# Optimization experiments

Hardware: AMD Instinct MI355X
Metric: run time of the kernel (lower is better)

Reference implementation:

```python
import jax, jax.numpy as jnp
import numpy as np

B, H, WD, C = 16, 96, 96, 256
WS, SH, NH = 6, 3, 8
N = WS * WS
ALPHA = (2 * 6) ** 0.25  # deepnorm alpha, n_layers=6
SCALE = (C // NH) ** 0.5  # faithful to source: head_dim**0.5 (not **-0.5)
EPS = 1e-5


def _rel_index(ws):
    coords = np.stack(np.meshgrid(np.arange(ws), np.arange(ws), indexing='ij'))  # (2,ws,ws)
    flat = coords.reshape(2, -1)
    rel = (flat[:, :, None] - flat[:, None, :]).transpose(1, 2, 0).copy()
    rel[..., 0] += ws - 1
    rel[..., 1] += ws - 1
    rel[..., 0] *= 2 * ws - 1
    return jnp.asarray(rel.sum(-1))  # (N,N) int


def _attn_mask(h, w, ws, sh):
    img = np.zeros((h, w))
    cnt = 0
    for hs in (slice(0, -ws), slice(-ws, -sh), slice(-sh, None)):
        for wsl in (slice(0, -ws), slice(-ws, -sh), slice(-sh, None)):
            img[hs, wsl] = cnt
            cnt += 1
    win = img.reshape(h // ws, ws, w // ws, ws).transpose(0, 2, 1, 3).reshape(-1, ws * ws)
    diff = win[:, None, :] - win[:, :, None]
    return jnp.asarray(np.where(diff != 0, -100.0, 0.0), jnp.float32)  # (nW,N,N)


def _ln(t, w, b):
    mu = jnp.mean(t, -1, keepdims=True)
    var = jnp.var(t, -1, keepdims=True)
    return (t - mu) * jax.lax.rsqrt(var + EPS) * w + b


def setup_inputs() -> dict:
    key = jax.random.key(0)
    ks = jax.random.split(key, 8)
    d = {
        'x': jax.random.normal(ks[0], (B, H * WD, C), jnp.float32),
        'qkv_w': jax.random.normal(ks[1], (C, 3 * C), jnp.float32) * 0.02,
        'qkv_b': jnp.zeros((3 * C,), jnp.float32),
        'bias_table': jax.random.normal(ks[2], ((2 * WS - 1) ** 2, NH), jnp.float32) * 0.02,
        'proj_w': jax.random.normal(ks[3], (C, C), jnp.float32) * 0.02,
        'proj_b': jnp.zeros((C,), jnp.float32),
        'norm1_w': jnp.ones((C,), jnp.float32),
        'norm1_b': jnp.zeros((C,), jnp.float32),
        'norm2_w': jnp.ones((C,), jnp.float32),
        'norm2_b': jnp.zeros((C,), jnp.float32),
        'fc1_w': jax.random.normal(ks[4], (C, 4 * C), jnp.float32) * 0.02,
        'fc1_b': jnp.zeros((4 * C,), jnp.float32),
        'fc2_w': jax.random.normal(ks[5], (4 * C, C), jnp.float32) * 0.02,
        'fc2_b': jnp.zeros((C,), jnp.float32),
    }
    return d


def reference(x, qkv_w, qkv_b, bias_table, proj_w, proj_b, norm1_w, norm1_b,
              norm2_w, norm2_b, fc1_w, fc1_b, fc2_w, fc2_b):
    hd = C // NH
    nW = (H // WS) * (WD // WS)
    shortcut = x  # (B, L, C), norm_before=False -> post-norm
    xs = x.reshape(B, H, WD, C)
    xs = jnp.roll(xs, (-SH, -SH), axis=(1, 2))  # cyclic shift
    # window partition -> (B*nW, N, C)
    xw = xs.reshape(B, H // WS, WS, WD // WS, WS, C).transpose(0, 1, 3, 2, 4, 5).reshape(B * nW, N, C)
    qkv = (xw @ qkv_w + qkv_b).reshape(B * nW, N, 3, NH, hd).transpose(2, 0, 3, 1, 4)
    q, k, v = qkv[0] * SCALE, qkv[1], qkv[2]
    attn = jnp.einsum('bhnd,bhmd->bhnm', q, k)  # (B*nW, H, N, N)
    bias = bias_table[_rel_index(WS).reshape(-1)].reshape(N, N, NH).transpose(2, 0, 1)
    attn = attn + bias[None]
    mask = _attn_mask(H, WD, WS, SH)  # (nW, N, N)
    attn = attn.reshape(B, nW, NH, N, N) + mask[None, :, None]
    attn = jax.nn.softmax(attn.reshape(B * nW, NH, N, N), axis=-1)
    out = jnp.einsum('bhnm,bhmd->bhnd', attn, v).transpose(0, 2, 1, 3).reshape(B * nW, N, C)
    out = out @ proj_w + proj_b
    # faithful buggy window_reverse: identity permute == plain reshape
    xs = out.reshape(B, H // WS, WS, WD // WS, WS, C).reshape(B, H, WD, C)
    xs = jnp.roll(xs, (SH, SH), axis=(1, 2))
    x1 = _ln(shortcut * ALPHA + xs.reshape(B, H * WD, C), norm1_w, norm1_b)
    hmid = jax.nn.gelu(x1 @ fc1_w + fc1_b, approximate=False)
    x2 = _ln(x1 * ALPHA + (hmid @ fc2_w + fc2_b), norm2_w, norm2_b)
    return x2
```

## Files before the change

kernel.cpp:

```cpp
#include <hip/hip_runtime.h>
#include <math.h>

typedef __bf16 bf16x8 __attribute__((ext_vector_type(8)));
typedef float f32x4 __attribute__((ext_vector_type(4)));

#define NTOK 147456
#define LTOK 9216
#define ALPHA 1.8612097182041991f
#define QSCALE 5.656854249492380196f
#define MFMA16(a,b,c) __builtin_amdgcn_mfma_f32_16x16x32_bf16((a),(b),(c),0,0,0)
#define SWB(row,kb) ((kb) ^ ((row)&7))

__device__ __forceinline__ float gelu_sig(float x) {
    const float e = __expf(-1.702f * x);
    return x * __builtin_amdgcn_rcpf(1.0f + e);
}

__device__ __forceinline__ void gll16(const void* g, void* l) {
    __builtin_amdgcn_global_load_lds(
        (const __attribute__((address_space(1))) void*)g,
        (__attribute__((address_space(3))) void*)l, 16, 0, 0);
}

__global__ __launch_bounds__(256) void k0_prep(
    const float* __restrict__ qkv_w, const float* __restrict__ proj_w,
    const float* __restrict__ fc1_w, const float* __restrict__ fc2_w,
    __bf16* __restrict__ qkvT, __bf16* __restrict__ projT,
    __bf16* __restrict__ w1T, __bf16* __restrict__ w2T)
{
    const int id = blockIdx.x * 256 + threadIdx.x;
    if (id < 196608) {
        const int o = id >> 8, k = id & 255;
        qkvT[id] = (__bf16)qkv_w[k * 768 + o];
    } else if (id < 262144) {
        const int i = id - 196608, o = i >> 8, k = i & 255;
        projT[i] = (__bf16)proj_w[k * 256 + o];
    } else if (id < 524288) {
        const int i = id - 262144, o = i >> 8, k = i & 255;
        w1T[i] = (__bf16)fc1_w[k * 1024 + o];
    } else {
        const int i = id - 524288, o = i >> 10, k = i & 1023;
        w2T[i] = (__bf16)fc2_w[k * 256 + o];
    }
}

__global__ __launch_bounds__(512, 4) void k1f_qkv_attn(
    const float* __restrict__ x, const __bf16* __restrict__ qkvT,
    const float* __restrict__ qkv_b, const float* __restrict__ bias_table,
    __bf16* __restrict__ attnout)
{
    __shared__ __attribute__((aligned(16))) char SM[81920];
    typedef __bf16 (*a256_t)[256];
    typedef __bf16 (*b32_t)[32];
    typedef __bf16 (*s64_t)[64];
    a256_t As = (a256_t)SM;
    b32_t  Bs = (b32_t)(SM + 24576);
    int* srcrow = (int*)(SM + 73728);

    const int t = threadIdx.x;
    const int wid = t >> 6, lane = t & 63;
    const int l15 = lane & 15, lg = lane >> 4;
    const int blk = blockIdx.x;
    const int win = blk & 255;
    const int wh = win >> 4, ww = win & 15;
    const int h = wid;

    if (t < 48) {
        int n = t; if (n > 35) n = 35;
        const int b = blk >> 8;
        const int gh = (wh * 6 + n / 6 + 3) % 96;
        const int gw = (ww * 6 + n % 6 + 3) % 96;
        srcrow[t] = b * LTOK + gh * 96 + gw;
    }
    __syncthreads();

    for (int o = t; o < 48 * 32; o += 512) {
        const int row = o >> 5, kb = o & 31;
        const float* src = x + (size_t)srcrow[row] * 256 + kb * 8;
        const float4 f0 = *(const float4*)src;
        const float4 f1 = *(const float4*)(src + 4);
        bf16x8 p;
        p[0] = (__bf16)f0.x; p[1] = (__bf16)f0.y; p[2] = (__bf16)f0.z; p[3] = (__bf16)f0.w;
        p[4] = (__bf16)f1.x; p[5] = (__bf16)f1.y; p[6] = (__bf16)f1.z; p[7] = (__bf16)f1.w;
        *(bf16x8*)&As[row][SWB(row, kb) * 8] = p;
    }

    const f32x4 fzero = {0.f, 0.f, 0.f, 0.f};
    f32x4 acc[3][3][2];
    #pragma unroll
    for (int nb = 0; nb < 3; ++nb)
        #pragma unroll
        for (int i = 0; i < 3; ++i)
            #pragma unroll
            for (int j = 0; j < 2; ++j) acc[nb][i][j] = fzero;

    for (int kc = 0; kc < 8; ++kc) {
        __syncthreads();
        #pragma unroll
        for (int i = 0; i < 6; ++i) {
            const int r0 = wid * 96 + i * 16;
            const int row = r0 + (lane >> 2), kbl = lane & 3;
            gll16(qkvT + (size_t)row * 256 + kc * 32 + ((kbl ^ (row & 3)) * 8),
                  &Bs[r0][0]);
        }
        __syncthreads();
        bf16x8 af[3];
        #pragma unroll
        for (int rt = 0; rt < 3; ++rt) {
            const int ar = rt * 16 + l15;
            const int kb = kc * 4 + lg;
            af[rt] = *(const bf16x8*)&As[ar][SWB(ar, kb) * 8];
        }
        #pragma unroll
        for (int nb = 0; nb < 3; ++nb)
            #pragma unroll
            for (int ct = 0; ct < 2; ++ct) {
                const int br = nb * 256 + h * 32 + ct * 16 + l15;
                const bf16x8 bfr = *(const bf16x8*)&Bs[br][((lg ^ (br & 3))) * 8];
                #pragma unroll
                for (int rt = 0; rt < 3; ++rt)
                    acc[nb][rt][ct] = MFMA16(af[rt], bfr, acc[nb][rt][ct]);
            }
    }
    __syncthreads();

    s64_t slab = (s64_t)(SM + wid * 10240);
    s64_t vT   = (s64_t)(SM + wid * 10240 + 6144);
    const size_t rowbase = (size_t)blk * 36;

    int i2_[3], j2_[3], g2_[3];
    #pragma unroll
    for (int ct = 0; ct < 3; ++ct) {
        const int m = ct * 16 + l15;
        const int mm = m < 36 ? m : 35;
        i2_[ct] = mm / 6; j2_[ct] = mm - i2_[ct] * 6;
        const int hg = (wh < 15) ? 0 : (i2_[ct] < 3 ? 1 : 2);
        const int wg = (ww < 15) ? 0 : (j2_[ct] < 3 ? 1 : 2);
        g2_[ct] = hg * 3 + wg;
    }

    #pragma unroll
    for (int ct = 0; ct < 2; ++ct) {
        const int dq = ct * 16 + l15;
        const float qb  = qkv_b[h * 32 + dq];
        const float kb2 = qkv_b[256 + h * 32 + dq];
        #pragma unroll
        for (int rt = 0; rt < 3; ++rt)
            #pragma unroll
            for (int q = 0; q < 4; ++q) {
                const int tok = rt * 16 + lg * 4 + q;
                const int c = (((dq >> 3) ^ (tok & 3)) * 8) + (dq & 7);
                slab[tok][c]      = (__bf16)((acc[0][rt][ct][q] + qb) * QSCALE);
                slab[tok][32 + c] = (__bf16)(acc[1][rt][ct][q] + kb2);
            }
    }

    bf16x8 aq[3], bk[3];
    #pragma unroll
    for (int rt = 0; rt < 3; ++rt) {
        const int ar = rt * 16 + l15;
        aq[rt] = *(const bf16x8*)&slab[ar][((lg ^ (ar & 3))) * 8];
        bk[rt] = *(const bf16x8*)&slab[ar][32 + ((lg ^ (ar & 3))) * 8];
    }
    f32x4 s[3][3];
    #pragma unroll
    for (int rt = 0; rt < 3; ++rt)
        #pragma unroll
        for (int ct = 0; ct < 3; ++ct)
            s[rt][ct] = MFMA16(aq[rt], bk[ct], fzero);

    float inv_[3][4];
    #pragma unroll
    for (int rt = 0; rt < 3; ++rt) {
        #pragma unroll
        for (int q = 0; q < 4; ++q) {
            const int n0 = rt * 16 + lg * 4 + q;
            const int nn = n0 < 36 ? n0 : 35;
            const int i1 = nn / 6, j1 = nn - i1 * 6;
            const int hg1 = (wh < 15) ? 0 : (i1 < 3 ? 1 : 2);
            const int wg1 = (ww < 15) ? 0 : (j1 < 3 ? 1 : 2);
            const int g1 = hg1 * 3 + wg1;
            #pragma unroll
            for (int ct = 0; ct < 3; ++ct) {
                const int m = ct * 16 + l15;
                float val;
                if (m < 36) {
                    val = s[rt][ct][q] + bias_table[((i1 - i2_[ct] + 5) * 11 + (j1 - j2_[ct] + 5)) * 8 + h];
                    if (g1 != g2_[ct]) val -= 100.0f;
                } else {
                    val = -1e30f;
                }
                s[rt][ct][q] = val;
            }
            float mx = fmaxf(fmaxf(s[rt][0][q], s[rt][1][q]), s[rt][2][q]);
            mx = fmaxf(mx, __shfl_xor(mx, 1, 16));
            mx = fmaxf(mx, __shfl_xor(mx, 2, 16));
            mx = fmaxf(mx, __shfl_xor(mx, 4, 16));
            mx = fmaxf(mx, __shfl_xor(mx, 8, 16));
            float sum = 0.f;
            #pragma unroll
            for (int ct = 0; ct < 3; ++ct) {
                const float e = __expf(s[rt][ct][q] - mx);
                s[rt][ct][q] = e;
                sum += e;
            }
            sum += __shfl_xor(sum, 1, 16);
            sum += __shfl_xor(sum, 2, 16);
            sum += __shfl_xor(sum, 4, 16);
            sum += __shfl_xor(sum, 8, 16);
            inv_[rt][q] = 1.0f / sum;
        }
    }

    #pragma unroll
    for (int rt = 0; rt < 3; ++rt)
        #pragma unroll
        for (int q = 0; q < 4; ++q) {
            const int row = rt * 16 + lg * 4 + q;
            #pragma unroll
            for (int ct = 0; ct < 3; ++ct) {
                const int m = ct * 16 + l15;
                slab[row][(((m >> 3) ^ (row & 7)) * 8) + (m & 7)] = (__bf16)s[rt][ct][q];
            }
            const int mz = 48 + l15;
            slab[row][(((mz >> 3) ^ (row & 7)) * 8) + (mz & 7)] = (__bf16)0.0f;
        }

    #pragma unroll
    for (int ct = 0; ct < 2; ++ct) {
        const int d = ct * 16 + l15;
        const float vb = qkv_b[512 + h * 32 + d];
        #pragma unroll
        for (int rt = 0; rt < 3; ++rt)
            #pragma unroll
            for (int q = 0; q < 4; ++q) {
                const int m = rt * 16 + lg * 4 + q;
                vT[d][(((m >> 3) ^ (d & 7)) * 8) + (m & 7)] = (__bf16)(acc[2][rt][ct][q] + vb);
            }
    }
    for (int z = lane; z < 512; z += 64) {
        const int d = z >> 4, m = 48 + (z & 15);
        vT[d][(((m >> 3) ^ (d & 7)) * 8) + (m & 7)] = (__bf16)0.0f;
    }

    f32x4 ov[3][2];
    #pragma unroll
    for (int rt = 0; rt < 3; ++rt)
        #pragma unroll
        for (int cd = 0; cd < 2; ++cd) ov[rt][cd] = fzero;
    #pragma unroll
    for (int kk = 0; kk < 2; ++kk) {
        bf16x8 pa[3], bv[2];
        #pragma unroll
        for (int rt = 0; rt < 3; ++rt) {
            const int ar = rt * 16 + l15;
            pa[rt] = *(const bf16x8*)&slab[ar][(((kk * 4 + lg) ^ (ar & 7))) * 8];
        }
        #pragma unroll
        for (int cd = 0; cd < 2; ++cd) {
            const int d = cd * 16 + l15;
            bv[cd] = *(const bf16x8*)&vT[d][(((kk * 4 + lg) ^ (d & 7))) * 8];
        }
        #pragma unroll
        for (int rt = 0; rt < 3; ++rt)
            #pragma unroll
            for (int cd = 0; cd < 2; ++cd)
                ov[rt][cd] = MFMA16(pa[rt], bv[cd], ov[rt][cd]);
    }

    #pragma unroll
    for (int rt = 0; rt < 3; ++rt)
        #pragma unroll
        for (int cd = 0; cd < 2; ++cd)
            #pragma unroll
            for (int q = 0; q < 4; ++q) {
                const int n = rt * 16 + lg * 4 + q;
                if (n < 36)
                    attnout[(rowbase + n) * 256 + h * 32 + cd * 16 + l15] =
                        (__bf16)(ov[rt][cd][q] * inv_[rt][q]);
            }
}

__global__ __launch_bounds__(512) void k2_proj_ln(
    const __bf16* __restrict__ attnout, const __bf16* __restrict__ projT,
    const float* __restrict__ proj_b, const float* __restrict__ x,
    const float* __restrict__ n1w, const float* __restrict__ n1b,
    __bf16* __restrict__ x1b)
{
    __shared__ __attribute__((aligned(16))) __bf16 As[128][64];
    __shared__ __attribute__((aligned(16))) __bf16 Bs[256][64];
    __shared__ float ps[128][4], ps2[128][4];
    const int t = threadIdx.x;
    const int wid = t >> 6, lane = t & 63;
    const int l15 = lane & 15, lg = lane >> 4;
    const int mb = blockIdx.x;
    const int wm = wid >> 2, wn = wid & 3;

    const f32x4 fzero = {0.f, 0.f, 0.f, 0.f};
    f32x4 acc[4][4];
    #pragma unroll
    for (int i = 0; i < 4; ++i)
        #pragma unroll
        for (int j = 0; j < 4; ++j) acc[i][j] = fzero;

    for (int kc = 0; kc < 4; ++kc) {
        __syncthreads();
        #pragma unroll
        for (int i = 0; i < 2; ++i) {
            const int r0 = wid * 16 + i * 8;
            const int row = r0 + (lane >> 3), kbl = lane & 7;
            gll16(attnout + (size_t)(mb * 128 + row) * 256 + kc * 64 + ((kbl ^ (row & 7)) * 8),
                  &As[r0][0]);
        }
        #pragma unroll
        for (int i = 0; i < 4; ++i) {
            const int r0 = wid * 32 + i * 8;
            const int row = r0 + (lane >> 3), kbl = lane & 7;
            gll16(projT + (size_t)row * 256 + kc * 64 + ((kbl ^ (row & 7)) * 8),
                  &Bs[r0][0]);
        }
        __syncthreads();
        #pragma unroll
        for (int kk = 0; kk < 2; ++kk) {
            bf16x8 af[4], bfr[4];
            #pragma unroll
            for (int rt = 0; rt < 4; ++rt) {
                const int ar = wm * 64 + rt * 16 + l15;
                af[rt] = *(const bf16x8*)&As[ar][((kk * 4 + lg) ^ (ar & 7)) * 8];
            }
            #pragma unroll
            for (int ct = 0; ct < 4; ++ct) {
                const int br = wn * 64 + ct * 16 + l15;
                bfr[ct] = *(const bf16x8*)&Bs[br][((kk * 4 + lg) ^ (br & 7)) * 8];
            }
            #pragma unroll
            for (int rt = 0; rt < 4; ++rt)
                #pragma unroll
                for (int ct = 0; ct < 4; ++ct)
                    acc[rt][ct] = MFMA16(af[rt], bfr[ct], acc[rt][ct]);
        }
    }

    int dtok_[4][4];
    #pragma unroll
    for (int rt = 0; rt < 4; ++rt) {
        #pragma unroll
        for (int q = 0; q < 4; ++q) {
            const int rowl = wm * 64 + rt * 16 + lg * 4 + q;
            const int tok = mb * 128 + rowl;
            const int b = tok / LTOK, l = tok % LTOK;
            const int hh = l / 96, wwp = l % 96;
            const int dtok = b * LTOK + ((hh + 3) % 96) * 96 + ((wwp + 3) % 96);
            dtok_[rt][q] = dtok;
            float s = 0.f, s2 = 0.f;
            #pragma unroll
            for (int ct = 0; ct < 4; ++ct) {
                const int col = wn * 64 + ct * 16 + l15;
                const float v = acc[rt][ct][q] + proj_b[col] + ALPHA * x[(size_t)dtok * 256 + col];
                acc[rt][ct][q] = v;
                s += v; s2 += v * v;
            }
            s  += __shfl_xor(s, 1, 16);  s += __shfl_xor(s, 2, 16);
            s  += __shfl_xor(s, 4, 16);  s += __shfl_xor(s, 8, 16);
            s2 += __shfl_xor(s2, 1, 16); s2 += __shfl_xor(s2, 2, 16);
            s2 += __shfl_xor(s2, 4, 16); s2 += __shfl_xor(s2, 8, 16);
            if (l15 == 0) { ps[rowl][wn] = s; ps2[rowl][wn] = s2; }
        }
    }
    __syncthreads();
    #pragma unroll
    for (int rt = 0; rt < 4; ++rt) {
        #pragma unroll
        for (int q = 0; q < 4; ++q) {
            const int rowl = wm * 64 + rt * 16 + lg * 4 + q;
            const float S  = ps[rowl][0] + ps[rowl][1] + ps[rowl][2] + ps[rowl][3];
            const float S2 = ps2[rowl][0] + ps2[rowl][1] + ps2[rowl][2] + ps2[rowl][3];
            const float mu = S * (1.0f / 256.0f);
            const float var = S2 * (1.0f / 256.0f) - mu * mu;
            const float rstd = rsqrtf(var + 1e-5f);
            __bf16* op = x1b + (size_t)dtok_[rt][q] * 256;
            #pragma unroll
            for (int ct = 0; ct < 4; ++ct) {
                const int col = wn * 64 + ct * 16 + l15;
                op[col] = (__bf16)((acc[rt][ct][q] - mu) * rstd * n1w[col] + n1b[col]);
            }
        }
    }
}

__global__ __launch_bounds__(512, 2) void k3f_mlp(
    const __bf16* __restrict__ x1b, const __bf16* __restrict__ w1T,
    const float* __restrict__ fc1_b, const __bf16* __restrict__ w2T,
    const float* __restrict__ fc2_b, const float* __restrict__ n2w,
    const float* __restrict__ n2b, float* __restrict__ out)
{
    __shared__ __attribute__((aligned(16))) __bf16 w1c[2][64][256];
    __shared__ __attribute__((aligned(16))) __bf16 w2c[2][256][64];
    __shared__ __attribute__((aligned(16))) __bf16 hs[128][72];
    __shared__ float ps[128][2], ps2[128][2];

    const int t = threadIdx.x;
    const int wid = t >> 6, lane = t & 63;
    const int l15 = lane & 15, lg = lane >> 4;
    const int rg = wid >> 1, chs = wid & 1;
    const int rowbase = blockIdx.x * 128 + rg * 32;

    bf16x8 af[2][8];
    #pragma unroll
    for (int rt = 0; rt < 2; ++rt)
        #pragma unroll
        for (int kk = 0; kk < 8; ++kk)
            af[rt][kk] = *(const bf16x8*)(x1b + (size_t)(rowbase + rt * 16 + l15) * 256 + kk * 32 + lg * 8);

    const f32x4 fzero = {0.f, 0.f, 0.f, 0.f};
    f32x4 acc2[2][8];
    #pragma unroll
    for (int i = 0; i < 2; ++i)
        #pragma unroll
        for (int j = 0; j < 8; ++j) acc2[i][j] = fzero;

    #define STAGE_W(b, c)                                                       \
    {                                                                           \
        _Pragma("unroll")                                                       \
        for (int i = 0; i < 4; ++i) {                                           \
            const int r0 = wid * 8 + i * 2;                                     \
            const int row = r0 + (lane >> 5);                                   \
            const int g = (lane & 31) ^ (row & 7);                              \
            gll16(w1T + (size_t)((c) * 64 + row) * 256 + g * 8, &w1c[b][r0][0]);\
        }                                                                       \
        _Pragma("unroll")                                                       \
        for (int i = 0; i < 4; ++i) {                                           \
            const int r0 = wid * 32 + i * 8;                                    \
            const int row = r0 + (lane >> 3);                                   \
            const int g = (lane & 7) ^ (row & 7);                               \
            gll16(w2T + (size_t)row * 1024 + (c) * 64 + g * 8, &w2c[b][r0][0]); \
        }                                                                       \
    }

    STAGE_W(0, 0);
    __syncthreads();

    for (int ch = 0; ch < 16; ++ch) {
        const int cur = ch & 1;
        if (ch < 15) STAGE_W(cur ^ 1, ch + 1);

        f32x4 acc1[2][2];
        #pragma unroll
        for (int i = 0; i < 2; ++i)
            #pragma unroll
            for (int j = 0; j < 2; ++j) acc1[i][j] = fzero;
        #pragma unroll
        for (int kk = 0; kk < 8; ++kk) {
            #pragma unroll
            for (int ct = 0; ct < 2; ++ct) {
                const int br = chs * 32 + ct * 16 + l15;
                const bf16x8 b = *(const bf16x8*)&w1c[cur][br][((kk * 4 + lg) ^ (br & 7)) * 8];
                #pragma unroll
                for (int rt = 0; rt < 2; ++rt)
                    acc1[rt][ct] = MFMA16(af[rt][kk], b, acc1[rt][ct]);
            }
        }
        #pragma unroll
        for (int ct = 0; ct < 2; ++ct) {
            const int hid = chs * 32 + ct * 16 + l15;
            const float b1v = fc1_b[ch * 64 + hid];
            #pragma unroll
            for (int rt = 0; rt < 2; ++rt)
                #pragma unroll
                for (int q = 0; q < 4; ++q) {
                    const int lrow = rt * 16 + lg * 4 + q;
                    hs[rg * 32 + lrow][((hid >> 3) ^ (lrow & 7)) * 8 + (hid & 7)] =
                        (__bf16)gelu_sig(acc1[rt][ct][q] + b1v);
                }
        }
        asm volatile("s_waitcnt lgkmcnt(0)" ::: "memory");
        __builtin_amdgcn_sched_barrier(0);
        __builtin_amdgcn_s_barrier();
        __builtin_amdgcn_sched_barrier(0);

        #pragma unroll
        for (int kk2 = 0; kk2 < 2; ++kk2) {
            bf16x8 a[2];
            #pragma unroll
            for (int rt = 0; rt < 2; ++rt) {
                const int grow = rg * 32 + rt * 16 + l15;
                a[rt] = *(const bf16x8*)&hs[grow][((kk2 * 4 + lg) ^ (l15 & 7)) * 8];
            }
            #pragma unroll
            for (int ct = 0; ct < 8; ++ct) {
                const int br = chs * 128 + ct * 16 + l15;
                const bf16x8 b = *(const bf16x8*)&w2c[cur][br][((kk2 * 4 + lg) ^ (br & 7)) * 8];
                #pragma unroll
                for (int rt = 0; rt < 2; ++rt)
                    acc2[rt][ct] = MFMA16(a[rt], b, acc2[rt][ct]);
            }
        }

        asm volatile("s_waitcnt vmcnt(0) lgkmcnt(0)" ::: "memory");
        __builtin_amdgcn_sched_barrier(0);
        __builtin_amdgcn_s_barrier();
        __builtin_amdgcn_sched_barrier(0);
    }

    #pragma unroll
    for (int rt = 0; rt < 2; ++rt) {
        #pragma unroll
        for (int q = 0; q < 4; ++q) {
            const int lrow = rt * 16 + lg * 4 + q;
            const int grow = rg * 32 + lrow;
            const size_t tok = (size_t)(blockIdx.x * 128 + grow);
            float s = 0.f, s2 = 0.f;
            #pragma unroll
            for (int ct = 0; ct < 8; ++ct) {
                const int col = chs * 128 + ct * 16 + l15;
                const float v = acc2[rt][ct][q] + fc2_b[col] + ALPHA * (float)x1b[tok * 256 + col];
                acc2[rt][ct][q] = v;
                s += v; s2 += v * v;
            }
            s  += __shfl_xor(s, 1, 16);  s += __shfl_xor(s, 2, 16);
            s  += __shfl_xor(s, 4, 16);  s += __shfl_xor(s, 8, 16);
            s2 += __shfl_xor(s2, 1, 16); s2 += __shfl_xor(s2, 2, 16);
            s2 += __shfl_xor(s2, 4, 16); s2 += __shfl_xor(s2, 8, 16);
            if (l15 == 0) { ps[grow][chs] = s; ps2[grow][chs] = s2; }
        }
    }
    __syncthreads();
    #pragma unroll
    for (int rt = 0; rt < 2; ++rt) {
        #pragma unroll
        for (int q = 0; q < 4; ++q) {
            const int lrow = rt * 16 + lg * 4 + q;
            const int grow = rg * 32 + lrow;
            const size_t tok = (size_t)(blockIdx.x * 128 + grow);
            const float S  = ps[grow][0] + ps[grow][1];
            const float S2 = ps2[grow][0] + ps2[grow][1];
            const float mu = S * (1.0f / 256.0f);
            const float var = S2 * (1.0f / 256.0f) - mu * mu;
            const float rstd = rsqrtf(var + 1e-5f);
            float* op = out + tok * 256;
            #pragma unroll
            for (int ct = 0; ct < 8; ++ct) {
                const int col = chs * 128 + ct * 16 + l15;
                op[col] = (acc2[rt][ct][q] - mu) * rstd * n2w[col] + n2b[col];
            }
        }
    }
    #undef STAGE_W
}

extern "C" void kernel_launch(void* const* d_in, const int* in_sizes, int n_in,
                              void* d_out, int out_size, void* d_ws, size_t ws_size,
                              hipStream_t stream)
{
    const float* x          = (const float*)d_in[0];
    const float* qkv_w      = (const float*)d_in[1];
    const float* qkv_b      = (const float*)d_in[2];
    const float* bias_table = (const float*)d_in[3];
    const float* proj_w     = (const float*)d_in[4];
    const float* proj_b     = (const float*)d_in[5];
    const float* n1w        = (const float*)d_in[6];
    const float* n1b        = (const float*)d_in[7];
    const float* n2w        = (const float*)d_in[8];
    const float* n2b        = (const float*)d_in[9];
    const float* fc1_w      = (const float*)d_in[10];
    const float* fc1_b      = (const float*)d_in[11];
    const float* fc2_w      = (const float*)d_in[12];
    const float* fc2_b      = (const float*)d_in[13];
    float* out = (float*)d_out;

    char* ws = (char*)d_ws;
    __bf16* x1b     = (__bf16*)ws;
    __bf16* attnout = (__bf16*)(ws + 75497472);
    __bf16* qkvT    = (__bf16*)(ws + 150994944);
    __bf16* projT   = (__bf16*)(ws + 151388160);
    __bf16* w1T     = (__bf16*)(ws + 151519232);
    __bf16* w2T     = (__bf16*)(ws + 152043520);

    k0_prep<<<3072, 256, 0, stream>>>(qkv_w, proj_w, fc1_w, fc2_w, qkvT, projT, w1T, w2T);
    k1f_qkv_attn<<<4096, 512, 0, stream>>>(x, qkvT, qkv_b, bias_table, attnout);
    k2_proj_ln<<<1152, 512, 0, stream>>>(attnout, projT, proj_b, x, n1w, n1b, x1b);
    k3f_mlp<<<1152, 512, 0, stream>>>(x1b, w1T, fc1_b, w2T, fc2_b, n2w, n2b, out);
}
```

Measured before the change: 677.4 us.

## Keep attention and MLP intermediates in registers via transposed MFMA operand layouts

```diff
diff --git a/kernel.cpp b/kernel.cpp
--- a/kernel.cpp
+++ b/kernel.cpp
@@ -2,14 +2,29 @@
 #include <math.h>
 
 typedef __bf16 bf16x8 __attribute__((ext_vector_type(8)));
-typedef float f32x4 __attribute__((ext_vector_type(4)));
+typedef __bf16 bf16x4 __attribute__((ext_vector_type(4)));
+typedef short  s16x4  __attribute__((ext_vector_type(4)));
+typedef float  f32x4  __attribute__((ext_vector_type(4)));
 
 #define NTOK 147456
 #define LTOK 9216
 #define ALPHA 1.8612097182041991f
 #define QSCALE 5.656854249492380196f
-#define MFMA16(a,b,c) __builtin_amdgcn_mfma_f32_16x16x32_bf16((a),(b),(c),0,0,0)
+#define MFMA32(a,b,c) __builtin_amdgcn_mfma_f32_16x16x32_bf16((a),(b),(c),0,0,0)
 #define SWB(row,kb) ((kb) ^ ((row)&7))
+
+__device__ __forceinline__ f32x4 MFMA16(bf16x4 a, bf16x4 b, f32x4 c) {
+#if __has_builtin(__builtin_amdgcn_mfma_f32_16x16x16bf16_1k)
+    return __builtin_amdgcn_mfma_f32_16x16x16bf16_1k(*(s16x4*)&a, *(s16x4*)&b, c, 0, 0, 0);
+#else
+    f32x4 d = c;
+    asm volatile("s_nop 1\n\ts_nop 1\n\t"
+                 "v_mfma_f32_16x16x16_bf16 %0, %1, %2, %0\n\t"
+                 "s_nop 7\n\ts_nop 7"
+                 : "+v"(d) : "v"(a), "v"(b));
+    return d;
+#endif
+}
 
 __device__ __forceinline__ float gelu_sig(float x) {
     const float e = __expf(-1.702f * x);
@@ -49,13 +64,13 @@
     const float* __restrict__ qkv_b, const float* __restrict__ bias_table,
     __bf16* __restrict__ attnout)
 {
-    __shared__ __attribute__((aligned(16))) char SM[81920];
+    __shared__ __attribute__((aligned(16))) char SM[77824];
     typedef __bf16 (*a256_t)[256];
     typedef __bf16 (*b32_t)[32];
-    typedef __bf16 (*s64_t)[64];
     a256_t As = (a256_t)SM;
     b32_t  Bs = (b32_t)(SM + 24576);
-    int* srcrow = (int*)(SM + 73728);
+    int*   srcrow = (int*)(SM + 73728);
+    float* bias_s = (float*)(SM + 73920);
 
     const int t = threadIdx.x;
     const int wid = t >> 6, lane = t & 63;
@@ -72,6 +87,7 @@
         const int gw = (ww * 6 + n % 6 + 3) % 96;
         srcrow[t] = b * LTOK + gh * 96 + gw;
     }
+    for (int o = t; o < 968; o += 512) bias_s[o] = bias_table[o];
     __syncthreads();
 
     for (int o = t; o < 48 * 32; o += 512) {
@@ -86,13 +102,11 @@
     }
 
     const f32x4 fzero = {0.f, 0.f, 0.f, 0.f};
-    f32x4 acc[3][3][2];
-    #pragma unroll
-    for (int nb = 0; nb < 3; ++nb)
-        #pragma unroll
-        for (int i = 0; i < 3; ++i)
-            #pragma unroll
-            for (int j = 0; j < 2; ++j) acc[nb][i][j] = fzero;
+    f32x4 accQ[2][3], accK[2][3], accV[2][3];
+    #pragma unroll
+    for (int c = 0; c < 2; ++c)
+        #pragma unroll
+        for (int r = 0; r < 3; ++r) { accQ[c][r] = fzero; accK[c][r] = fzero; accV[c][r] = fzero; }
 
     for (int kc = 0; kc < 8; ++kc) {
         __syncthreads();
@@ -112,173 +126,129 @@
             af[rt] = *(const bf16x8*)&As[ar][SWB(ar, kb) * 8];
         }
         #pragma unroll
-        for (int nb = 0; nb < 3; ++nb)
-            #pragma unroll
-            for (int ct = 0; ct < 2; ++ct) {
-                const int br = nb * 256 + h * 32 + ct * 16 + l15;
-                const bf16x8 bfr = *(const bf16x8*)&Bs[br][((lg ^ (br & 3))) * 8];
-                #pragma unroll
-                for (int rt = 0; rt < 3; ++rt)
-                    acc[nb][rt][ct] = MFMA16(af[rt], bfr, acc[nb][rt][ct]);
-            }
-    }
-    __syncthreads();
-
-    s64_t slab = (s64_t)(SM + wid * 10240);
-    s64_t vT   = (s64_t)(SM + wid * 10240 + 6144);
+        for (int ct = 0; ct < 2; ++ct) {
+            const int brq = h * 32 + ct * 16 + l15;
+            const bf16x8 bq = *(const bf16x8*)&Bs[brq][((lg ^ (brq & 3))) * 8];
+            const int brk = 256 + brq;
+            const bf16x8 bk = *(const bf16x8*)&Bs[brk][((lg ^ (brk & 3))) * 8];
+            const int brv = 512 + brq;
+            const bf16x8 bv = *(const bf16x8*)&Bs[brv][((lg ^ (brv & 3))) * 8];
+            #pragma unroll
+            for (int rt = 0; rt < 3; ++rt) {
+                accQ[ct][rt] = MFMA32(bq, af[rt], accQ[ct][rt]);
+                accK[ct][rt] = MFMA32(bk, af[rt], accK[ct][rt]);
+                accV[ct][rt] = MFMA32(af[rt], bv, accV[ct][rt]);
+            }
+        }
+    }
+
+    bf16x4 qf[3][2], kf[3][2], vf[2][3];
+    #pragma unroll
+    for (int dh = 0; dh < 2; ++dh) {
+        #pragma unroll
+        for (int q = 0; q < 4; ++q) {
+            const float qb = qkv_b[h * 32 + dh * 16 + lg * 4 + q];
+            const float kb = qkv_b[256 + h * 32 + dh * 16 + lg * 4 + q];
+            #pragma unroll
+            for (int rt = 0; rt < 3; ++rt) {
+                qf[rt][dh][q] = (__bf16)((accQ[dh][rt][q] + qb) * QSCALE);
+                kf[rt][dh][q] = (__bf16)(accK[dh][rt][q] + kb);
+            }
+        }
+    }
+    #pragma unroll
+    for (int cd = 0; cd < 2; ++cd) {
+        const float vb = qkv_b[512 + h * 32 + cd * 16 + l15];
+        #pragma unroll
+        for (int c3 = 0; c3 < 3; ++c3)
+            #pragma unroll
+            for (int q = 0; q < 4; ++q)
+                vf[cd][c3][q] = (__bf16)(accV[cd][c3][q] + vb);
+    }
+
+    f32x4 s[3][3];
+    #pragma unroll
+    for (int qt = 0; qt < 3; ++qt)
+        #pragma unroll
+        for (int c3 = 0; c3 < 3; ++c3) {
+            f32x4 acc = MFMA16(kf[c3][0], qf[qt][0], fzero);
+            s[qt][c3] = MFMA16(kf[c3][1], qf[qt][1], acc);
+        }
+
+    int i2_[3][4], j2_[3][4], g2_[3][4];
+    #pragma unroll
+    for (int c3 = 0; c3 < 3; ++c3)
+        #pragma unroll
+        for (int q = 0; q < 4; ++q) {
+            const int kt = c3 * 16 + lg * 4 + q;
+            const int kk2 = kt < 36 ? kt : 35;
+            i2_[c3][q] = kk2 / 6; j2_[c3][q] = kk2 - i2_[c3][q] * 6;
+            g2_[c3][q] = ((wh < 15) ? 0 : (i2_[c3][q] < 3 ? 1 : 2)) * 3
+                       + ((ww < 15) ? 0 : (j2_[c3][q] < 3 ? 1 : 2));
+        }
+
+    bf16x4 pa[3][3];
+    #pragma unroll
+    for (int qt = 0; qt < 3; ++qt) {
+        const int qtok = qt * 16 + l15;
+        const int nn = qtok < 36 ? qtok : 35;
+        const int i1 = nn / 6, j1 = nn - i1 * 6;
+        const int g1 = ((wh < 15) ? 0 : (i1 < 3 ? 1 : 2)) * 3
+                     + ((ww < 15) ? 0 : (j1 < 3 ? 1 : 2));
+        float vals[3][4];
+        float mx = -1e30f;
+        #pragma unroll
+        for (int c3 = 0; c3 < 3; ++c3)
+            #pragma unroll
+            for (int q = 0; q < 4; ++q) {
+                const int kt = c3 * 16 + lg * 4 + q;
+                float v;
+                if (kt < 36) {
+                    v = s[qt][c3][q]
+                      + bias_s[((i1 - i2_[c3][q] + 5) * 11 + (j1 - j2_[c3][q] + 5)) * 8 + h];
+                    if (g1 != g2_[c3][q]) v -= 100.0f;
+                } else {
+                    v = -1e30f;
+                }
+                vals[c3][q] = v;
+                mx = fmaxf(mx, v);
+            }
+        mx = fmaxf(mx, __shfl_xor(mx, 16));
+        mx = fmaxf(mx, __shfl_xor(mx, 32));
+        float sum = 0.f;
+        #pragma unroll
+        for (int c3 = 0; c3 < 3; ++c3)
+            #pragma unroll
+            for (int q = 0; q < 4; ++q) {
+                const float e = __expf(vals[c3][q] - mx);
+                vals[c3][q] = e;
+                sum += e;
+            }
+        sum += __shfl_xor(sum, 16);
+        sum += __shfl_xor(sum, 32);
+        const float inv = 1.0f / sum;
+        #pragma unroll
+        for (int c3 = 0; c3 < 3; ++c3)
+            #pragma unroll
+            for (int q = 0; q < 4; ++q)
+                pa[qt][c3][q] = (__bf16)(vals[c3][q] * inv);
+    }
+
     const size_t rowbase = (size_t)blk * 36;
-
-    int i2_[3], j2_[3], g2_[3];
-    #pragma unroll
-    for (int ct = 0; ct < 3; ++ct) {
-        const int m = ct * 16 + l15;
-        const int mm = m < 36 ? m : 35;
-        i2_[ct] = mm / 6; j2_[ct] = mm - i2_[ct] * 6;
-        const int hg = (wh < 15) ? 0 : (i2_[ct] < 3 ? 1 : 2);
-        const int wg = (ww < 15) ? 0 : (j2_[ct] < 3 ? 1 : 2);
-        g2_[ct] = hg * 3 + wg;
-    }
-
-    #pragma unroll
-    for (int ct = 0; ct < 2; ++ct) {
-        const int dq = ct * 16 + l15;
-        const float qb  = qkv_b[h * 32 + dq];
-        const float kb2 = qkv_b[256 + h * 32 + dq];
-        #pragma unroll
-        for (int rt = 0; rt < 3; ++rt)
+    #pragma unroll
+    for (int qt = 0; qt < 3; ++qt)
+        #pragma unroll
+        for (int cd = 0; cd < 2; ++cd) {
+            f32x4 o = MFMA16(pa[qt][0], vf[cd][0], fzero);
+            o = MFMA16(pa[qt][1], vf[cd][1], o);
+            o = MFMA16(pa[qt][2], vf[cd][2], o);
             #pragma unroll
             for (int q = 0; q < 4; ++q) {
-                const int tok = rt * 16 + lg * 4 + q;
-                const int c = (((dq >> 3) ^ (tok & 3)) * 8) + (dq & 7);
-                slab[tok][c]      = (__bf16)((acc[0][rt][ct][q] + qb) * QSCALE);
-                slab[tok][32 + c] = (__bf16)(acc[1][rt][ct][q] + kb2);
-            }
-    }
-
-    bf16x8 aq[3], bk[3];
-    #pragma unroll
-    for (int rt = 0; rt < 3; ++rt) {
-        const int ar = rt * 16 + l15;
-        aq[rt] = *(const bf16x8*)&slab[ar][((lg ^ (ar & 3))) * 8];
-        bk[rt] = *(const bf16x8*)&slab[ar][32 + ((lg ^ (ar & 3))) * 8];
-    }
-    f32x4 s[3][3];
-    #pragma unroll
-    for (int rt = 0; rt < 3; ++rt)
-        #pragma unroll
-        for (int ct = 0; ct < 3; ++ct)
-            s[rt][ct] = MFMA16(aq[rt], bk[ct], fzero);
-
-    float inv_[3][4];
-    #pragma unroll
-    for (int rt = 0; rt < 3; ++rt) {
-        #pragma unroll
-        for (int q = 0; q < 4; ++q) {
-            const int n0 = rt * 16 + lg * 4 + q;
-            const int nn = n0 < 36 ? n0 : 35;
-            const int i1 = nn / 6, j1 = nn - i1 * 6;
-            const int hg1 = (wh < 15) ? 0 : (i1 < 3 ? 1 : 2);
-            const int wg1 = (ww < 15) ? 0 : (j1 < 3 ? 1 : 2);
-            const int g1 = hg1 * 3 + wg1;
-            #pragma unroll
-            for (int ct = 0; ct < 3; ++ct) {
-                const int m = ct * 16 + l15;
-                float val;
-                if (m < 36) {
-                    val = s[rt][ct][q] + bias_table[((i1 - i2_[ct] + 5) * 11 + (j1 - j2_[ct] + 5)) * 8 + h];
-                    if (g1 != g2_[ct]) val -= 100.0f;
-                } else {
-                    val = -1e30f;
-                }
-                s[rt][ct][q] = val;
-            }
-            float mx = fmaxf(fmaxf(s[rt][0][q], s[rt][1][q]), s[rt][2][q]);
-            mx = fmaxf(mx, __shfl_xor(mx, 1, 16));
-            mx = fmaxf(mx, __shfl_xor(mx, 2, 16));
-            mx = fmaxf(mx, __shfl_xor(mx, 4, 16));
-            mx = fmaxf(mx, __shfl_xor(mx, 8, 16));
-            float sum = 0.f;
-            #pragma unroll
-            for (int ct = 0; ct < 3; ++ct) {
-                const float e = __expf(s[rt][ct][q] - mx);
-                s[rt][ct][q] = e;
-                sum += e;
-            }
-            sum += __shfl_xor(sum, 1, 16);
-            sum += __shfl_xor(sum, 2, 16);
-            sum += __shfl_xor(sum, 4, 16);
-            sum += __shfl_xor(sum, 8, 16);
-            inv_[rt][q] = 1.0f / sum;
-        }
-    }
-
-    #pragma unroll
-    for (int rt = 0; rt < 3; ++rt)
-        #pragma unroll
-        for (int q = 0; q < 4; ++q) {
-            const int row = rt * 16 + lg * 4 + q;
-            #pragma unroll
-            for (int ct = 0; ct < 3; ++ct) {
-                const int m = ct * 16 + l15;
-                slab[row][(((m >> 3) ^ (row & 7)) * 8) + (m & 7)] = (__bf16)s[rt][ct][q];
-            }
-            const int mz = 48 + l15;
-            slab[row][(((mz >> 3) ^ (row & 7)) * 8) + (mz & 7)] = (__bf16)0.0f;
-        }
-
-    #pragma unroll
-    for (int ct = 0; ct < 2; ++ct) {
-        const int d = ct * 16 + l15;
-        const float vb = qkv_b[512 + h * 32 + d];
-        #pragma unroll
-        for (int rt = 0; rt < 3; ++rt)
-            #pragma unroll
-            for (int q = 0; q < 4; ++q) {
-                const int m = rt * 16 + lg * 4 + q;
-                vT[d][(((m >> 3) ^ (d & 7)) * 8) + (m & 7)] = (__bf16)(acc[2][rt][ct][q] + vb);
-            }
-    }
-    for (int z = lane; z < 512; z += 64) {
-        const int d = z >> 4, m = 48 + (z & 15);
-        vT[d][(((m >> 3) ^ (d & 7)) * 8) + (m & 7)] = (__bf16)0.0f;
-    }
-
-    f32x4 ov[3][2];
-    #pragma unroll
-    for (int rt = 0; rt < 3; ++rt)
-        #pragma unroll
-        for (int cd = 0; cd < 2; ++cd) ov[rt][cd] = fzero;
-    #pragma unroll
-    for (int kk = 0; kk < 2; ++kk) {
-        bf16x8 pa[3], bv[2];
-        #pragma unroll
-        for (int rt = 0; rt < 3; ++rt) {
-            const int ar = rt * 16 + l15;
-            pa[rt] = *(const bf16x8*)&slab[ar][(((kk * 4 + lg) ^ (ar & 7))) * 8];
-        }
-        #pragma unroll
-        for (int cd = 0; cd < 2; ++cd) {
-            const int d = cd * 16 + l15;
-            bv[cd] = *(const bf16x8*)&vT[d][(((kk * 4 + lg) ^ (d & 7))) * 8];
-        }
-        #pragma unroll
-        for (int rt = 0; rt < 3; ++rt)
-            #pragma unroll
-            for (int cd = 0; cd < 2; ++cd)
-                ov[rt][cd] = MFMA16(pa[rt], bv[cd], ov[rt][cd]);
-    }
-
-    #pragma unroll
-    for (int rt = 0; rt < 3; ++rt)
-        #pragma unroll
-        for (int cd = 0; cd < 2; ++cd)
-            #pragma unroll
-            for (int q = 0; q < 4; ++q) {
-                const int n = rt * 16 + lg * 4 + q;
+                const int n = qt * 16 + lg * 4 + q;
                 if (n < 36)
-                    attnout[(rowbase + n) * 256 + h * 32 + cd * 16 + l15] =
-                        (__bf16)(ov[rt][cd][q] * inv_[rt][q]);
-            }
+                    attnout[(rowbase + n) * 256 + h * 32 + cd * 16 + l15] = (__bf16)o[q];
+            }
+        }
 }
 
 __global__ __launch_bounds__(512) void k2_proj_ln(
@@ -337,7 +307,7 @@
             for (int rt = 0; rt < 4; ++rt)
                 #pragma unroll
                 for (int ct = 0; ct < 4; ++ct)
-                    acc[rt][ct] = MFMA16(af[rt], bfr[ct], acc[rt][ct]);
+                    acc[rt][ct] = MFMA32(af[rt], bfr[ct], acc[rt][ct]);
         }
     }
 
@@ -396,7 +366,6 @@
 {
     __shared__ __attribute__((aligned(16))) __bf16 w1c[2][64][256];
     __shared__ __attribute__((aligned(16))) __bf16 w2c[2][256][64];
-    __shared__ __attribute__((aligned(16))) __bf16 hs[128][72];
     __shared__ float ps[128][2], ps2[128][2];
 
     const int t = threadIdx.x;
@@ -407,10 +376,10 @@
 
     bf16x8 af[2][8];
     #pragma unroll
-    for (int rt = 0; rt < 2; ++rt)
+    for (int tt = 0; tt < 2; ++tt)
         #pragma unroll
         for (int kk = 0; kk < 8; ++kk)
-            af[rt][kk] = *(const bf16x8*)(x1b + (size_t)(rowbase + rt * 16 + l15) * 256 + kk * 32 + lg * 8);
+            af[tt][kk] = *(const bf16x8*)(x1b + (size_t)(rowbase + tt * 16 + l15) * 256 + kk * 32 + lg * 8);
 
     const f32x4 fzero = {0.f, 0.f, 0.f, 0.f};
     f32x4 acc2[2][8];
@@ -444,77 +413,65 @@
         const int cur = ch & 1;
         if (ch < 15) STAGE_W(cur ^ 1, ch + 1);
 
-        f32x4 acc1[2][2];
-        #pragma unroll
-        for (int i = 0; i < 2; ++i)
+        f32x4 acc1[4][2];
+        #pragma unroll
+        for (int i = 0; i < 4; ++i)
             #pragma unroll
             for (int j = 0; j < 2; ++j) acc1[i][j] = fzero;
         #pragma unroll
         for (int kk = 0; kk < 8; ++kk) {
             #pragma unroll
-            for (int ct = 0; ct < 2; ++ct) {
-                const int br = chs * 32 + ct * 16 + l15;
-                const bf16x8 b = *(const bf16x8*)&w1c[cur][br][((kk * 4 + lg) ^ (br & 7)) * 8];
+            for (int ht = 0; ht < 4; ++ht) {
+                const int hr = ht * 16 + l15;
+                const bf16x8 aW = *(const bf16x8*)&w1c[cur][hr][((kk * 4 + lg) ^ (hr & 7)) * 8];
                 #pragma unroll
-                for (int rt = 0; rt < 2; ++rt)
-                    acc1[rt][ct] = MFMA16(af[rt][kk], b, acc1[rt][ct]);
-            }
-        }
-        #pragma unroll
-        for (int ct = 0; ct < 2; ++ct) {
-            const int hid = chs * 32 + ct * 16 + l15;
-            const float b1v = fc1_b[ch * 64 + hid];
-            #pragma unroll
-            for (int rt = 0; rt < 2; ++rt)
+                for (int tt = 0; tt < 2; ++tt)
+                    acc1[ht][tt] = MFMA32(aW, af[tt][kk], acc1[ht][tt]);
+            }
+        }
+
+        bf16x4 a16[2][4];
+        #pragma unroll
+        for (int ht = 0; ht < 4; ++ht) {
+            float bq[4];
+            #pragma unroll
+            for (int q = 0; q < 4; ++q)
+                bq[q] = fc1_b[ch * 64 + ht * 16 + lg * 4 + q];
+            #pragma unroll
+            for (int tt = 0; tt < 2; ++tt)
                 #pragma unroll
-                for (int q = 0; q < 4; ++q) {
-                    const int lrow = rt * 16 + lg * 4 + q;
-                    hs[rg * 32 + lrow][((hid >> 3) ^ (lrow & 7)) * 8 + (hid & 7)] =
-                        (__bf16)gelu_sig(acc1[rt][ct][q] + b1v);
-                }
-        }
-        asm volatile("s_waitcnt lgkmcnt(0)" ::: "memory");
-        __builtin_amdgcn_sched_barrier(0);
-        __builtin_amdgcn_s_barrier();
-        __builtin_amdgcn_sched_barrier(0);
-
-        #pragma unroll
-        for (int kk2 = 0; kk2 < 2; ++kk2) {
-            bf16x8 a[2];
-            #pragma unroll
-            for (int rt = 0; rt < 2; ++rt) {
-                const int grow = rg * 32 + rt * 16 + l15;
-                a[rt] = *(const bf16x8*)&hs[grow][((kk2 * 4 + lg) ^ (l15 & 7)) * 8];
-            }
+                for (int q = 0; q < 4; ++q)
+                    a16[tt][ht][q] = (__bf16)gelu_sig(acc1[ht][tt][q] + bq[q]);
+        }
+
+        #pragma unroll
+        for (int ht = 0; ht < 4; ++ht) {
             #pragma unroll
             for (int ct = 0; ct < 8; ++ct) {
                 const int br = chs * 128 + ct * 16 + l15;
-                const bf16x8 b = *(const bf16x8*)&w2c[cur][br][((kk2 * 4 + lg) ^ (br & 7)) * 8];
+                const bf16x4 bW = *(const bf16x4*)&w2c[cur][br]
+                    [((ht * 2 + (lg >> 1)) ^ (br & 7)) * 8 + (lg & 1) * 4];
                 #pragma unroll
-                for (int rt = 0; rt < 2; ++rt)
-                    acc2[rt][ct] = MFMA16(a[rt], b, acc2[rt][ct]);
-            }
-        }
-
-        asm volatile("s_waitcnt vmcnt(0) lgkmcnt(0)" ::: "memory");
-        __builtin_amdgcn_sched_barrier(0);
-        __builtin_amdgcn_s_barrier();
-        __builtin_amdgcn_sched_barrier(0);
-    }
-
-    #pragma unroll
-    for (int rt = 0; rt < 2; ++rt) {
+                for (int tt = 0; tt < 2; ++tt)
+                    acc2[tt][ct] = MFMA16(a16[tt][ht], bW, acc2[tt][ct]);
+            }
+        }
+
+        __syncthreads();
+    }
+
+    #pragma unroll
+    for (int tt = 0; tt < 2; ++tt) {
         #pragma unroll
         for (int q = 0; q < 4; ++q) {
-            const int lrow = rt * 16 + lg * 4 + q;
-            const int grow = rg * 32 + lrow;
+            const int grow = rg * 32 + tt * 16 + lg * 4 + q;
             const size_t tok = (size_t)(blockIdx.x * 128 + grow);
             float s = 0.f, s2 = 0.f;
             #pragma unroll
             for (int ct = 0; ct < 8; ++ct) {
                 const int col = chs * 128 + ct * 16 + l15;
-                const float v = acc2[rt][ct][q] + fc2_b[col] + ALPHA * (float)x1b[tok * 256 + col];
-                acc2[rt][ct][q] = v;
+                const float v = acc2[tt][ct][q] + fc2_b[col] + ALPHA * (float)x1b[tok * 256 + col];
+                acc2[tt][ct][q] = v;
                 s += v; s2 += v * v;
             }
             s  += __shfl_xor(s, 1, 16);  s += __shfl_xor(s, 2, 16);
@@ -526,11 +483,10 @@
     }
     __syncthreads();
     #pragma unroll
-    for (int rt = 0; rt < 2; ++rt) {
+    for (int tt = 0; tt < 2; ++tt) {
         #pragma unroll
         for (int q = 0; q < 4; ++q) {
-            const int lrow = rt * 16 + lg * 4 + q;
-            const int grow = rg * 32 + lrow;
+            const int grow = rg * 32 + tt * 16 + lg * 4 + q;
             const size_t tok = (size_t)(blockIdx.x * 128 + grow);
             const float S  = ps[grow][0] + ps[grow][1];
             const float S2 = ps2[grow][0] + ps2[grow][1];
@@ -541,7 +497,7 @@
             #pragma unroll
             for (int ct = 0; ct < 8; ++ct) {
                 const int col = chs * 128 + ct * 16 + l15;
-                op[col] = (acc2[rt][ct][q] - mu) * rstd * n2w[col] + n2b[col];
+                op[col] = (acc2[tt][ct][q] - mu) * rstd * n2w[col] + n2b[col];
             }
         }
     }
```

Measured after the change: 733.8 us. 8.3% more time.
